# Kernel optimization log

Hardware: AMD Instinct MI355X
Metric: run time of the kernel (lower is better)

## Reference

```python
import jax, jax.numpy as jnp
import numpy as np

HIDDEN = 128
SIGMA_D = 0.2
SIGMA_A = 15.0
ANGLE_K = 10
FACTOR_A = 180.0 / (SIGMA_A * np.pi)


def _div_term():
    half = HIDDEN // 2
    return jnp.exp(jnp.arange(half, dtype=jnp.float32) * (-np.log(10000.0) / half))


def _sinusoid(x):
    # x: float tensor of (integer-valued) indices; returns x.shape + (HIDDEN,)
    pos = x[..., None].astype(jnp.float32)
    dt = _div_term()
    s = jnp.sin(pos * dt)
    c = jnp.cos(pos * dt)
    # interleave: even channels sin, odd channels cos
    return jnp.stack([s, c], axis=-1).reshape(x.shape + (HIDDEN,))


def setup_inputs() -> dict:
    key = jax.random.key(0)
    k1, k2, k3, k4, k5 = jax.random.split(key, 5)
    B, N = 2, 1024
    scale = 1.0 / np.sqrt(HIDDEN)
    points = jax.random.normal(k1, (B, N, 3), dtype=jnp.float32)
    Wd = jax.random.normal(k2, (HIDDEN, HIDDEN), dtype=jnp.float32) * scale
    bd = jax.random.normal(k3, (HIDDEN,), dtype=jnp.float32) * scale
    Wa = jax.random.normal(k4, (HIDDEN, HIDDEN), dtype=jnp.float32) * scale
    ba = jax.random.normal(k5, (HIDDEN,), dtype=jnp.float32) * scale
    return {"points": points, "Wd": Wd, "bd": bd, "Wa": Wa, "ba": ba}


def _single(pts, Wd, bd, Wa, ba):
    # pts: (N, 3)
    n = pts.shape[0]
    diff = pts[:, None, :] - pts[None, :, :]            # (N, N, 3)
    dists = jnp.sqrt(jnp.sum(diff * diff, axis=-1))      # (N, N)
    idx_d = jnp.clip(jnp.round(dists / SIGMA_D), 0.0, 255.0)
    # k nearest neighbours (smallest distances, incl. self)
    _, nn = jax.lax.top_k(-dists, ANGLE_K)               # (N, K)
    vec = pts[nn] - pts[:, None, :]                      # (N, K, 3)
    vnorm = jnp.linalg.norm(vec, axis=-1, keepdims=True)
    unit = vec / (vnorm + 1e-8)
    cos_ang = jnp.clip(jnp.einsum('nkd,nld->nkl', unit, unit), -1.0, 1.0)
    angles = jnp.arccos(cos_ang)                         # (N, K, K)
    idx_a = jnp.clip(jnp.round(angles * FACTOR_A), 0.0, 255.0)
    # indices computed under no_grad in the original
    idx_d = jax.lax.stop_gradient(idx_d)
    idx_a = jax.lax.stop_gradient(idx_a)

    embed_d = _sinusoid(idx_d)                           # (N, N, C)
    embed_d = jnp.mean(embed_d @ Wd.T + bd, axis=1)      # (N, C)

    embed_a = _sinusoid(idx_a)                           # (N, K, K, C)
    embed_a = embed_a @ Wa.T + ba
    embed_a = jnp.max(embed_a.reshape(n, -1, HIDDEN), axis=1)  # (N, C)
    return embed_d + embed_a


def reference(points, Wd, bd, Wa, ba):
    return jax.vmap(_single, in_axes=(0, None, None, None, None))(points, Wd, bd, Wa, ba)
```

## Files before the change

kernel.cpp:

```cpp
#include <hip/hip_runtime.h>
#include <hip/hip_bf16.h>

#define NPTS 1024
#define HID 128
#define KNN 10
#define PPB 2
#define FLT_MAX_ 3.402823466e+38f

__global__ __launch_bounds__(512) void gse_build(
    const float* __restrict__ Wd, const float* __restrict__ bd,
    const float* __restrict__ Wa, const float* __restrict__ ba,
    const float* __restrict__ pts, int nP,
    float* __restrict__ Td, float* __restrict__ Ta, float4* __restrict__ P4) {
    const int blk = blockIdx.x;
    const int tid = threadIdx.x;

    {
        const int idx = blk * 8 + tid;
        if (tid < 8 && idx < nP) {
            P4[idx] = make_float4(pts[idx * 3 + 0], pts[idx * 3 + 1],
                                  pts[idx * 3 + 2], 0.0f);
        }
    }

    __shared__ float S[HID];
    __shared__ float part[512];
    const bool isA = (blk >= 256);
    const int v = isA ? blk - 256 : blk;
    const int c = tid & 127;
    const int seg = tid >> 7;

    if (tid < HID) {
        const int m = tid >> 1;
        const float dtm = expf((float)m * (float)(-9.210340371976184 / 64.0));
        const float arg = (float)v * dtm;
        S[tid] = (tid & 1) ? cosf(arg) : sinf(arg);
    }
    __syncthreads();

    const float* W = isA ? Wa : Wd;
    const float* wrow = W + c * HID + seg * 32;
    const float* srow = S + seg * 32;
    float acc = 0.0f;
    #pragma unroll
    for (int h = 0; h < 32; h += 4) {
        const float4 wv = *reinterpret_cast<const float4*>(wrow + h);
        acc += srow[h] * wv.x + srow[h + 1] * wv.y + srow[h + 2] * wv.z + srow[h + 3] * wv.w;
    }
    part[tid] = acc;
    __syncthreads();

    if (tid < HID) {
        const float s = (part[c] + part[c + 128]) + (part[c + 256] + part[c + 384]);
        if (isA) Ta[v * HID + c] = s + ba[c];
        else     Td[v * HID + c] = (s + bd[c]) * (1.0f / (float)NPTS);
    }
}

__global__ __launch_bounds__(512, 8) void gse_main2(
    const float4* __restrict__ P4,
    const float* __restrict__ Td,
    const float* __restrict__ Ta,
    float* __restrict__ out) {
    const int tid = threadIdx.x;
    const int pt  = tid >> 8;
    const int t   = tid & 255;
    const int lane = tid & 63;
    const int w   = (tid >> 6) & 3;
    const int gid = blockIdx.x * PPB + pt;

    const int b = gid >> 10;
    const int i = gid & 1023;
    const float4* P = P4 + (size_t)b * NPTS;

    __shared__ int h4[PPB][4][256];
    __shared__ unsigned long long cand[PPB][64];
    __shared__ int nn[PPB][KNN];
    __shared__ float uxs[PPB][KNN], uys[PPB][KNN], uzs[PPB][KNN];
    __shared__ float sums[PPB][256], mxs[PPB][256];
    __shared__ unsigned amask_s[PPB];
    __shared__ int ccnt[PPB];
    __shared__ int meta_s[PPB];

    {
        int* hf = (int*)h4[pt];
        hf[t] = 0; hf[t + 256] = 0; hf[t + 512] = 0; hf[t + 768] = 0;
    }
    if (t == 0) { amask_s[pt] = 0u; ccnt[pt] = 0; }
    const float4 p = P[i];
    __syncthreads();

    float d4[4];
    int q4[4];
    const int jb = w * 256;
    #pragma unroll
    for (int s = 0; s < 4; ++s) {
        const int j = jb + s * 64 + lane;
        const float4 q = P[j];
        const float dx = p.x - q.x;
        const float dy = p.y - q.y;
        const float dz = p.z - q.z;
        const float dd = sqrtf(dx * dx + dy * dy + dz * dz);
        d4[s] = dd;
        float qq = rintf(dd / 0.2f);
        qq = fminf(fmaxf(qq, 0.0f), 255.0f);
        q4[s] = (int)qq;
        atomicAdd(&h4[pt][w][q4[s]], 1);
    }
    __syncthreads();

    const int hsum = h4[pt][0][t] + h4[pt][1][t] + h4[pt][2][t] + h4[pt][3][t];
    h4[pt][0][t] = hsum;
    __syncthreads();
    const int* hist = h4[pt][0];

    if (w == 0) {
        int cum = hist[lane];
        #pragma unroll
        for (int off = 1; off < 64; off <<= 1) {
            const int n_ = __shfl_up(cum, off);
            if (lane >= off) cum += n_;
        }
        const unsigned long long bal = __ballot(cum >= KNN);
        const unsigned long long nz0 = __ballot(hist[lane] != 0);
        const unsigned long long nz1 = __ballot(hist[64 + lane] != 0);
        const unsigned long long nz2 = __ballot(hist[128 + lane] != 0);
        const unsigned long long nz3 = __ballot(hist[192 + lane] != 0);
        int maxbin;
        if (nz3)      maxbin = 192 + 63 - __clzll((long long)nz3);
        else if (nz2) maxbin = 128 + 63 - __clzll((long long)nz2);
        else if (nz1) maxbin = 64 + 63 - __clzll((long long)nz1);
        else          maxbin = 63 - __clzll((long long)nz0);
        int b10 = 0, c = 0;
        if (bal) { b10 = __ffsll(bal) - 1; c = __shfl(cum, b10); }
        const int fast = (bal != 0ull && c <= 64) ? 1 : 0;
        if (lane == 0) {
            meta_s[pt] = (b10 & 0xff) | ((fast ? c : 0) << 8)
                       | ((maxbin & 0xff) << 16) | (fast << 30);
        }
    }
    __syncthreads();
    const int meta = meta_s[pt];
    const int b10 = meta & 0xff;
    const int c = (meta >> 8) & 0xff;
    const int maxbin = (meta >> 16) & 0xff;
    const bool fast = ((meta >> 30) & 1) != 0;

    if (fast) {
        #pragma unroll
        for (int s = 0; s < 4; ++s) {
            const bool pred = (q4[s] <= b10);
            const unsigned long long m = __ballot(pred);
            if (m) {
                int base = 0;
                if (lane == 0) base = atomicAdd(&ccnt[pt], __popcll(m));
                base = __shfl(base, 0);
                if (pred) {
                    const int pos = base + (int)__popcll(m & ((1ull << lane) - 1ull));
                    const int idx = jb + s * 64 + lane;
                    cand[pt][pos] = ((unsigned long long)__float_as_uint(d4[s]) << 32)
                                  | (unsigned)idx;
                }
            }
        }
        __syncthreads();
        if (t < c) {
            const unsigned long long my = cand[pt][t];
            int rank = 0;
            #pragma unroll 8
            for (int pp = 0; pp < c; ++pp) {
                rank += (cand[pt][pp] < my) ? 1 : 0;
            }
            if (rank < KNN) nn[pt][rank] = (int)(my & 0xffffffffu);
        }
        __syncthreads();
    } else {
        unsigned valid = 0xfu;
        unsigned long long keep = 0;
        for (int r = 0; r < KNN; ++r) {
            float bv = FLT_MAX_;
            int bi = 0x7fffffff;
            #pragma unroll
            for (int s = 0; s < 4; ++s) {
                if (valid & (1u << s)) {
                    const float v_ = d4[s];
                    const int id_ = jb + s * 64 + lane;
                    if (v_ < bv || (v_ == bv && id_ < bi)) { bv = v_; bi = id_; }
                }
            }
            #pragma unroll
            for (int off = 32; off > 0; off >>= 1) {
                const float ov = __shfl_xor(bv, off);
                const int oi = __shfl_xor(bi, off);
                if (ov < bv || (ov == bv && oi < bi)) { bv = ov; bi = oi; }
            }
            const int loc = bi - jb;
            if (loc >= 0 && loc < 256 && lane == (loc & 63)) valid &= ~(1u << (loc >> 6));
            if (lane == r) keep = ((unsigned long long)__float_as_uint(bv) << 32)
                                | (unsigned)bi;
        }
        if (lane < KNN) cand[pt][w * KNN + lane] = keep;
        __syncthreads();
        if (t < 4 * KNN) {
            const unsigned long long my = cand[pt][t];
            int rank = 0;
            for (int pp = 0; pp < 4 * KNN; ++pp) {
                rank += (cand[pt][pp] < my) ? 1 : 0;
            }
            if (rank < KNN) nn[pt][rank] = (int)(my & 0xffffffffu);
        }
        __syncthreads();
    }

    if (t < KNN) {
        const float4 qn = P[nn[pt][t]];
        const float vx = qn.x - p.x;
        const float vy = qn.y - p.y;
        const float vz = qn.z - p.z;
        const float den = sqrtf(vx * vx + vy * vy + vz * vz) + 1e-8f;
        uxs[pt][t] = vx / den; uys[pt][t] = vy / den; uzs[pt][t] = vz / den;
    }
    __syncthreads();

    if (t < KNN * KNN) {
        const int k = t / KNN, l = t % KNN;
        float cc = uxs[pt][k] * uxs[pt][l] + uys[pt][k] * uys[pt][l]
                 + uzs[pt][k] * uzs[pt][l];
        cc = fminf(fmaxf(cc, -1.0f), 1.0f);
        const float ang = acosf(cc);
        float q = rintf(ang * (float)(180.0 / (15.0 * M_PI)));
        q = fminf(fmaxf(q, 0.0f), 15.0f);
        atomicOr(&amask_s[pt], 1u << (int)q);
    }
    __syncthreads();

    const unsigned am = amask_s[pt];
    const int c7 = t & 127;
    const int half = t >> 7;
    float s = 0.0f;
    const float* tdc = Td + c7;
    #pragma unroll 4
    for (int v = half; v <= maxbin; v += 2) {
        s += (float)hist[v] * tdc[v * HID];
    }
    float mx = -FLT_MAX_;
    const float* tac = Ta + c7;
    #pragma unroll
    for (int v = 0; v < 8; ++v) {
        const int vv = half * 8 + v;
        const float tv = tac[vv * HID];
        if (am & (1u << vv)) mx = fmaxf(mx, tv);
    }
    sums[pt][t] = s;
    mxs[pt][t] = mx;
    __syncthreads();
    if (t < HID) {
        out[(size_t)gid * HID + t] =
            (sums[pt][t] + sums[pt][t + 128]) + fmaxf(mxs[pt][t], mxs[pt][t + 128]);
    }
}

__global__ __launch_bounds__(256, 8) void gse_main(
    const float4* __restrict__ P4,
    const float* __restrict__ Td,
    const float* __restrict__ Ta,
    float* __restrict__ out) {
    const int gid = blockIdx.x;
    const int b = gid >> 10;
    const int i = gid & 1023;
    const float4* P = P4 + (size_t)b * NPTS;
    const int tid = threadIdx.x;
    const int lane = tid & 63;
    const int w = tid >> 6;

    __shared__ int h4[4][256];
    __shared__ unsigned long long cand[64];
    __shared__ int nn[KNN];
    __shared__ float uxs[KNN], uys[KNN], uzs[KNN];
    __shared__ float sums[256], mxs[256];
    __shared__ unsigned amask_s;
    __shared__ int ccnt;
    __shared__ int meta_s;

    {
        int* hf = (int*)h4;
        hf[tid] = 0; hf[tid + 256] = 0; hf[tid + 512] = 0; hf[tid + 768] = 0;
    }
    if (tid == 0) { amask_s = 0u; ccnt = 0; }
    const float4 p = P[i];
    __syncthreads();

    float d4[4];
    int q4[4];
    const int jb = w * 256;
    #pragma unroll
    for (int s = 0; s < 4; ++s) {
        const int j = jb + s * 64 + lane;
        const float4 q = P[j];
        const float dx = p.x - q.x;
        const float dy = p.y - q.y;
        const float dz = p.z - q.z;
        const float dd = sqrtf(dx * dx + dy * dy + dz * dz);
        d4[s] = dd;
        float qq = rintf(dd / 0.2f);
        qq = fminf(fmaxf(qq, 0.0f), 255.0f);
        q4[s] = (int)qq;
        atomicAdd(&h4[w][q4[s]], 1);
    }
    __syncthreads();

    const int hsum = h4[0][tid] + h4[1][tid] + h4[2][tid] + h4[3][tid];
    h4[0][tid] = hsum;
    __syncthreads();
    const int* hist = h4[0];

    if (w == 0) {
        int cum = hist[lane];
        #pragma unroll
        for (int off = 1; off < 64; off <<= 1) {
            const int n_ = __shfl_up(cum, off);
            if (lane >= off) cum += n_;
        }
        const unsigned long long bal = __ballot(cum >= KNN);
        const unsigned long long nz0 = __ballot(hist[lane] != 0);
        const unsigned long long nz1 = __ballot(hist[64 + lane] != 0);
        const unsigned long long nz2 = __ballot(hist[128 + lane] != 0);
        const unsigned long long nz3 = __ballot(hist[192 + lane] != 0);
        int maxbin;
        if (nz3)      maxbin = 192 + 63 - __clzll((long long)nz3);
        else if (nz2) maxbin = 128 + 63 - __clzll((long long)nz2);
        else if (nz1) maxbin = 64 + 63 - __clzll((long long)nz1);
        else          maxbin = 63 - __clzll((long long)nz0);
        int b10 = 0, c = 0;
        if (bal) { b10 = __ffsll(bal) - 1; c = __shfl(cum, b10); }
        const int fast = (bal != 0ull && c <= 64) ? 1 : 0;
        if (lane == 0) {
            meta_s = (b10 & 0xff) | ((fast ? c : 0) << 8)
                   | ((maxbin & 0xff) << 16) | (fast << 30);
        }
    }
    __syncthreads();
    const int meta = meta_s;
    const int b10 = meta & 0xff;
    const int c = (meta >> 8) & 0xff;
    const int maxbin = (meta >> 16) & 0xff;
    const bool fast = ((meta >> 30) & 1) != 0;

    if (fast) {
        #pragma unroll
        for (int s = 0; s < 4; ++s) {
            const bool pred = (q4[s] <= b10);
            const unsigned long long m = __ballot(pred);
            if (m) {
                int base = 0;
                if (lane == 0) base = atomicAdd(&ccnt, __popcll(m));
                base = __shfl(base, 0);
                if (pred) {
                    const int pos = base + (int)__popcll(m & ((1ull << lane) - 1ull));
                    const int idx = jb + s * 64 + lane;
                    cand[pos] = ((unsigned long long)__float_as_uint(d4[s]) << 32)
                              | (unsigned)idx;
                }
            }
        }
        __syncthreads();
        if (tid < c) {
            const unsigned long long my = cand[tid];
            int rank = 0;
            #pragma unroll 8
            for (int pp = 0; pp < c; ++pp) rank += (cand[pp] < my) ? 1 : 0;
            if (rank < KNN) nn[rank] = (int)(my & 0xffffffffu);
        }
        __syncthreads();
    } else {
        unsigned valid = 0xfu;
        unsigned long long keep = 0;
        for (int r = 0; r < KNN; ++r) {
            float bv = FLT_MAX_;
            int bi = 0x7fffffff;
            #pragma unroll
            for (int s = 0; s < 4; ++s) {
                if (valid & (1u << s)) {
                    const float v_ = d4[s];
                    const int id_ = jb + s * 64 + lane;
                    if (v_ < bv || (v_ == bv && id_ < bi)) { bv = v_; bi = id_; }
                }
            }
            #pragma unroll
            for (int off = 32; off > 0; off >>= 1) {
                const float ov = __shfl_xor(bv, off);
                const int oi = __shfl_xor(bi, off);
                if (ov < bv || (ov == bv && oi < bi)) { bv = ov; bi = oi; }
            }
            const int loc = bi - jb;
            if (loc >= 0 && loc < 256 && lane == (loc & 63)) valid &= ~(1u << (loc >> 6));
            if (lane == r) keep = ((unsigned long long)__float_as_uint(bv) << 32)
                                | (unsigned)bi;
        }
        if (lane < KNN) cand[w * KNN + lane] = keep;
        __syncthreads();
        if (tid < 4 * KNN) {
            const unsigned long long my = cand[tid];
            int rank = 0;
            for (int pp = 0; pp < 4 * KNN; ++pp) rank += (cand[pp] < my) ? 1 : 0;
            if (rank < KNN) nn[rank] = (int)(my & 0xffffffffu);
        }
        __syncthreads();
    }

    if (tid < KNN) {
        const float4 qn = P[nn[tid]];
        const float vx = qn.x - p.x;
        const float vy = qn.y - p.y;
        const float vz = qn.z - p.z;
        const float den = sqrtf(vx * vx + vy * vy + vz * vz) + 1e-8f;
        uxs[tid] = vx / den; uys[tid] = vy / den; uzs[tid] = vz / den;
    }
    __syncthreads();

    if (tid < KNN * KNN) {
        const int k = tid / KNN, l = tid % KNN;
        float cc = uxs[k] * uxs[l] + uys[k] * uys[l] + uzs[k] * uzs[l];
        cc = fminf(fmaxf(cc, -1.0f), 1.0f);
        const float ang = acosf(cc);
        float q = rintf(ang * (float)(180.0 / (15.0 * M_PI)));
        q = fminf(fmaxf(q, 0.0f), 15.0f);
        atomicOr(&amask_s, 1u << (int)q);
    }
    __syncthreads();

    const unsigned am = amask_s;
    const int c7 = tid & 127;
    const int half = tid >> 7;
    float s = 0.0f;
    const float* tdc = Td + c7;
    #pragma unroll 4
    for (int v = half; v <= maxbin; v += 2) {
        s += (float)hist[v] * tdc[v * HID];
    }
    float mx = -FLT_MAX_;
    const float* tac = Ta + c7;
    #pragma unroll
    for (int v = 0; v < 8; ++v) {
        const int vv = half * 8 + v;
        const float tv = tac[vv * HID];
        if (am & (1u << vv)) mx = fmaxf(mx, tv);
    }
    sums[tid] = s;
    mxs[tid] = mx;
    __syncthreads();
    if (tid < HID) {
        out[(size_t)gid * HID + tid] =
            (sums[tid] + sums[tid + 128]) + fmaxf(mxs[tid], mxs[tid + 128]);
    }
}

extern "C" void kernel_launch(void* const* d_in, const int* in_sizes, int n_in,
                              void* d_out, int out_size, void* d_ws, size_t ws_size,
                              hipStream_t stream) {
    const float* pts = (const float*)d_in[0];
    const float* Wd  = (const float*)d_in[1];
    const float* bd  = (const float*)d_in[2];
    const float* Wa  = (const float*)d_in[3];
    const float* ba  = (const float*)d_in[4];
    float* out = (float*)d_out;

    const int B = in_sizes[0] / (NPTS * 3);
    const int nP = B * NPTS;

    float* Td = (float*)d_ws;
    float* Ta = Td + 256 * HID;
    float4* P4 = (float4*)(Ta + 16 * HID);

    gse_build<<<272, 512, 0, stream>>>(Wd, bd, Wa, ba, pts, nP, Td, Ta, P4);
    if (nP % PPB == 0) {
        gse_main2<<<nP / PPB, PPB * 256, 0, stream>>>(P4, Td, Ta, out);
    } else {
        gse_main<<<nP, 256, 0, stream>>>(P4, Td, Ta, out);
    }
}
```

Measured before the change: 20.13 us.

## Pack four points per block and fuse unit-vector step into angle pass

Raises the points handled per block from two to four, giving 1024-thread blocks and half as many launches' worth of blocks. Drops the separate per-neighbour unit-vector stage and its shared arrays plus one barrier; each of the 100 angle threads now reloads both neighbour points and recomputes their norms. Also makes the point-packing loop in the build kernel grid-stride so it covers every point. The larger blocks lower scheduling granularity but can reduce occupancy and raise barrier cost, and the recomputation adds redundant loads and divides.

```diff
diff --git a/kernel.cpp b/kernel.cpp
--- a/kernel.cpp
+++ b/kernel.cpp
@@ -4,7 +4,7 @@
 #define NPTS 1024
 #define HID 128
 #define KNN 10
-#define PPB 2
+#define PPB 4
 #define FLT_MAX_ 3.402823466e+38f
 
 __global__ __launch_bounds__(512) void gse_build(
@@ -15,9 +15,8 @@
     const int blk = blockIdx.x;
     const int tid = threadIdx.x;
 
-    {
-        const int idx = blk * 8 + tid;
-        if (tid < 8 && idx < nP) {
+    if (tid < 8) {
+        for (int idx = blk * 8 + tid; idx < nP; idx += 272 * 8) {
             P4[idx] = make_float4(pts[idx * 3 + 0], pts[idx * 3 + 1],
                                   pts[idx * 3 + 2], 0.0f);
         }
@@ -57,7 +56,7 @@
     }
 }
 
-__global__ __launch_bounds__(512, 8) void gse_main2(
+__global__ __launch_bounds__(1024, 8) void gse_main4(
     const float4* __restrict__ P4,
     const float* __restrict__ Td,
     const float* __restrict__ Ta,
@@ -76,7 +75,6 @@
     __shared__ int h4[PPB][4][256];
     __shared__ unsigned long long cand[PPB][64];
     __shared__ int nn[PPB][KNN];
-    __shared__ float uxs[PPB][KNN], uys[PPB][KNN], uzs[PPB][KNN];
     __shared__ float sums[PPB][256], mxs[PPB][256];
     __shared__ unsigned amask_s[PPB];
     __shared__ int ccnt[PPB];
@@ -212,20 +210,20 @@
         __syncthreads();
     }
 
-    if (t < KNN) {
-        const float4 qn = P[nn[pt][t]];
-        const float vx = qn.x - p.x;
-        const float vy = qn.y - p.y;
-        const float vz = qn.z - p.z;
-        const float den = sqrtf(vx * vx + vy * vy + vz * vz) + 1e-8f;
-        uxs[pt][t] = vx / den; uys[pt][t] = vy / den; uzs[pt][t] = vz / den;
-    }
-    __syncthreads();
-
     if (t < KNN * KNN) {
         const int k = t / KNN, l = t % KNN;
-        float cc = uxs[pt][k] * uxs[pt][l] + uys[pt][k] * uys[pt][l]
-                 + uzs[pt][k] * uzs[pt][l];
+        const int jk = nn[pt][k], jl = nn[pt][l];
+        const float4 qk = P[jk];
+        const float4 ql = P[jl];
+        const float kx = qk.x - p.x;
+        const float ky = qk.y - p.y;
+        const float kz = qk.z - p.z;
+        const float dk = sqrtf(kx * kx + ky * ky + kz * kz) + 1e-8f;
+        const float lx = ql.x - p.x;
+        const float ly = ql.y - p.y;
+        const float lz = ql.z - p.z;
+        const float dl = sqrtf(lx * lx + ly * ly + lz * lz) + 1e-8f;
+        float cc = (kx / dk) * (lx / dl) + (ky / dk) * (ly / dl) + (kz / dk) * (lz / dl);
         cc = fminf(fmaxf(cc, -1.0f), 1.0f);
         const float ang = acosf(cc);
         float q = rintf(ang * (float)(180.0 / (15.0 * M_PI)));
@@ -276,7 +274,6 @@
     __shared__ int h4[4][256];
     __shared__ unsigned long long cand[64];
     __shared__ int nn[KNN];
-    __shared__ float uxs[KNN], uys[KNN], uzs[KNN];
     __shared__ float sums[256], mxs[256];
     __shared__ unsigned amask_s;
     __shared__ int ccnt;
@@ -408,19 +405,20 @@
         __syncthreads();
     }
 
-    if (tid < KNN) {
-        const float4 qn = P[nn[tid]];
-        const float vx = qn.x - p.x;
-        const float vy = qn.y - p.y;
-        const float vz = qn.z - p.z;
-        const float den = sqrtf(vx * vx + vy * vy + vz * vz) + 1e-8f;
-        uxs[tid] = vx / den; uys[tid] = vy / den; uzs[tid] = vz / den;
-    }
-    __syncthreads();
-
     if (tid < KNN * KNN) {
         const int k = tid / KNN, l = tid % KNN;
-        float cc = uxs[k] * uxs[l] + uys[k] * uys[l] + uzs[k] * uzs[l];
+        const int jk = nn[k], jl = nn[l];
+        const float4 qk = P[jk];
+        const float4 ql = P[jl];
+        const float kx = qk.x - p.x;
+        const float ky = qk.y - p.y;
+        const float kz = qk.z - p.z;
+        const float dk = sqrtf(kx * kx + ky * ky + kz * kz) + 1e-8f;
+        const float lx = ql.x - p.x;
+        const float ly = ql.y - p.y;
+        const float lz = ql.z - p.z;
+        const float dl = sqrtf(lx * lx + ly * ly + lz * lz) + 1e-8f;
+        float cc = (kx / dk) * (lx / dl) + (ky / dk) * (ly / dl) + (kz / dk) * (lz / dl);
         cc = fminf(fmaxf(cc, -1.0f), 1.0f);
         const float ang = acosf(cc);
         float q = rintf(ang * (float)(180.0 / (15.0 * M_PI)));
@@ -474,7 +472,7 @@
 
     gse_build<<<272, 512, 0, stream>>>(Wd, bd, Wa, ba, pts, nP, Td, Ta, P4);
     if (nP % PPB == 0) {
-        gse_main2<<<nP / PPB, PPB * 256, 0, stream>>>(P4, Td, Ta, out);
+        gse_main4<<<nP / PPB, PPB * 256, 0, stream>>>(P4, Td, Ta, out);
     } else {
         gse_main<<<nP, 256, 0, stream>>>(P4, Td, Ta, out);
     }
```

Result: slower. 21.83 us (+8.4%).
